# Kernel optimization log

Measured on AMD Instinct MI355X. Metric: run time of the kernel, lower is better.

The kernel has to match this reference:

```python
import jax, jax.numpy as jnp
import numpy as np

B, T, U = 64, 400, 64
V, E, H = 80, 128, 400
M, K = 10, 20  # attention mixtures, output mixtures


def _lstm_cell(x, h, c, W_ih, W_hh, b_ih, b_hh):
    g = x @ W_ih.T + b_ih + h @ W_hh.T + b_hh
    i, f, gg, o = jnp.split(g, 4, axis=-1)
    c_new = jax.nn.sigmoid(f) * c + jax.nn.sigmoid(i) * jnp.tanh(gg)
    h_new = jax.nn.sigmoid(o) * jnp.tanh(c_new)
    return h_new, c_new


def setup_inputs() -> dict:
    key = jax.random.key(0)
    ks = jax.random.split(key, 16)
    s = 0.05
    inp = {
        'strokes': jax.random.normal(ks[0], (B, T, 3), jnp.float32),
        'chars': jax.random.randint(ks[1], (B, U), 0, V, jnp.int32),
        'chars_mask': jnp.ones((B, U), jnp.float32),
        'emb': jax.random.normal(ks[2], (V, E)) * s,
        # layer_0: input 3+E
        'W_ih0': jax.random.normal(ks[3], (4 * H, 3 + E)) * s,
        'W_hh0': jax.random.normal(ks[4], (4 * H, H)) * s,
        'b_ih0': jnp.zeros((4 * H,)), 'b_hh0': jnp.zeros((4 * H,)),
        # layer_n[0], layer_n[1]: input 3+E+H
        'W_ih1': jax.random.normal(ks[5], (4 * H, 3 + E + H)) * s,
        'W_hh1': jax.random.normal(ks[6], (4 * H, H)) * s,
        'b_ih1': jnp.zeros((4 * H,)), 'b_hh1': jnp.zeros((4 * H,)),
        'W_ih2': jax.random.normal(ks[7], (4 * H, 3 + E + H)) * s,
        'W_hh2': jax.random.normal(ks[8], (4 * H, H)) * s,
        'b_ih2': jnp.zeros((4 * H,)), 'b_hh2': jnp.zeros((4 * H,)),
        # Gaussian attention linear: H -> 3M
        'Wa': jax.random.normal(ks[9], (3 * M, H)) * s,
        'ba': jnp.zeros((3 * M,)),
        # output linear: 3H -> 6K+1
        'Wo': jax.random.normal(ks[10], (6 * K + 1, 3 * H)) * s,
        'bo': jnp.zeros((6 * K + 1,)),
        # learned initial states
        'h0': jnp.zeros((3, H)), 'c0': jnp.zeros((3, H)),
        'w0': jnp.zeros((E,)), 'k0': jnp.zeros((M,)),
    }
    return inp


def _forward(strokes, chars, chars_mask, emb, W_ih0, W_hh0, b_ih0, b_hh0,
             W_ih1, W_hh1, b_ih1, b_hh1, W_ih2, W_hh2, b_ih2, b_hh2,
             Wa, ba, Wo, bo, h0, c0, w0, k0):
    ctx = emb[chars] * chars_mask[:, :, None]            # (B,U,E)
    u = jnp.arange(U, dtype=jnp.float32)                 # (U,)
    bsz = strokes.shape[0]

    def attn(h_t, k_tm1):
        p = jnp.exp(h_t @ Wa.T + ba)                     # (B,3M)
        alpha, beta, kappa = jnp.split(p, 3, axis=-1)    # (B,M) each
        kappa = kappa + k_tm1
        # phi: (B,U)
        phi = jnp.sum(alpha[:, None, :] * jnp.exp(-beta[:, None, :]
                      * (kappa[:, None, :] - u[None, :, None]) ** 2), axis=-1)
        w = jnp.sum(phi[:, :, None] * ctx, axis=1)       # (B,E)
        return w, kappa

    bc = lambda v: jnp.broadcast_to(v, (bsz,) + v.shape)
    carry0 = (bc(h0[0]), bc(h0[1]), bc(h0[2]),
              bc(c0[0]), bc(c0[1]), bc(c0[2]), bc(w0), bc(k0))

    def step(carry, x_t):
        h0_, h1_, h2_, c0_, c1_, c2_, w_, k_ = carry
        # layer_0
        hA, cA = _lstm_cell(jnp.concatenate([x_t, w_], 1), h0_, c0_,
                            W_ih0, W_hh0, b_ih0, b_hh0)
        w_n, k_n = attn(hA, k_)
        # faithful replication of source's buggy layer_n loop (j starts at 0):
        # j=0: input uses h_tm1[-1] (slot2), prev state = slot1, writes slot0
        n0h, n0c = _lstm_cell(jnp.concatenate([x_t, w_n, h2_], 1), h1_, c1_,
                              W_ih1, W_hh1, b_ih1, b_hh1)
        # j=1: input uses h_tm1[0] (just written), prev state = slot2, writes slot1
        n1h, n1c = _lstm_cell(jnp.concatenate([x_t, w_n, n0h], 1), h2_, c2_,
                              W_ih2, W_hh2, b_ih2, b_hh2)
        # slot2 never updated; output uses [slot0, slot1, slot2]
        out = jnp.concatenate([n0h, n1h, h2_], 1) @ Wo.T + bo
        return (n0h, n1h, h2_, n0c, n1c, c2_, w_n, k_n), out

    _, outs = jax.lax.scan(step, carry0, jnp.swapaxes(strokes, 0, 1))
    out = jnp.swapaxes(outs, 0, 1)                       # (B,T,6K+1)

    mu, log_sigma, pi, rho_raw, eos = jnp.split(
        out, [2 * K, 4 * K, 5 * K, 6 * K], axis=-1)
    sigma = jnp.exp(log_sigma).reshape(out.shape[0], out.shape[1], K, 2)
    mu = mu.reshape(out.shape[0], out.shape[1], K, 2)
    rho = jnp.tanh(rho_raw)                              # (B,T,K)
    log_pi = jax.nn.log_softmax(pi, axis=-1)

    x = strokes[:, :, None, :2]                          # (B,T,1,2)
    t = (x - mu) / sigma                                 # (B,T,K,2)
    Z = jnp.sum(t ** 2, -1) - 2.0 * rho * t[..., 0] * t[..., 1]
    num = -Z / (2.0 * (1.0 - rho ** 2))
    denom = (np.log(2 * np.pi) + jnp.sum(jnp.log(sigma), -1)
             + 0.5 * jnp.log(1.0 - rho ** 2))
    log_N = num - denom
    stroke_loss = jnp.mean(-jax.nn.logsumexp(log_pi + log_N, axis=-1))

    y = strokes[:, :, 2:3]
    z = eos
    eos_loss = jnp.mean(jnp.maximum(z, 0.0) - z * y
                        + jnp.log1p(jnp.exp(-jnp.abs(z))))
    return jnp.stack([stroke_loss, eos_loss])


def reference(strokes, chars, chars_mask, emb, W_ih0, W_hh0, b_ih0, b_hh0,
              W_ih1, W_hh1, b_ih1, b_hh1, W_ih2, W_hh2, b_ih2, b_hh2,
              Wa, ba, Wo, bo, h0, c0, w0, k0):
    return _forward(strokes, chars, chars_mask, emb, W_ih0, W_hh0, b_ih0,
                    b_hh0, W_ih1, W_hh1, b_ih1, b_hh1, W_ih2, W_hh2, b_ih2,
                    b_hh2, Wa, ba, Wo, bo, h0, c0, w0, k0)
```

## Files before the change

kernel.cpp:

```cpp
#include <hip/hip_runtime.h>
#include <hip/hip_bf16.h>


#define B_ 64
#define T_ 400
#define U_ 64
#define E_ 128
#define H_ 400
#define M_ 10
#define NO_ 121

#define NBLK 100
#define NTHR 512

constexpr size_t OF_WS2  = 128;
constexpr size_t OF_KS   = OF_WS2 + 64*128;
constexpr size_t OF_N0H  = OF_KS + 640;
constexpr size_t OF_N0C  = OF_N0H + 25600;
constexpr size_t OF_N1H  = OF_N0C + 25600;
constexpr size_t OF_N1C  = OF_N1H + 25600;
constexpr size_t OF_HA   = OF_N1C + 25600;
constexpr size_t OF_B0   = OF_HA + 25600;
constexpr size_t OF_B1   = OF_B0 + 1600;
constexpr size_t OF_B2   = OF_B1 + 1600;
constexpr size_t OF_OB   = OF_B2 + 1600;
constexpr size_t OF_XT   = OF_OB + 128;
constexpr size_t OF_CTX  = OF_XT + (size_t)T_*3*64;
constexpr size_t OF_A0   = OF_CTX + (size_t)64*64*128;
constexpr size_t OF_A1   = OF_A0 + (size_t)T_*64*400/2;
constexpr size_t WS_FLOATS = OF_A1 + (size_t)T_*64*400/2;

__device__ __forceinline__ float sigf(float x) { return 1.f/(1.f + expf(-x)); }

__device__ __forceinline__ void gbar(unsigned* cnt, unsigned* gen, unsigned tgt) {
  __syncthreads();
  if (threadIdx.x == 0) {
    unsigned prev = __hip_atomic_fetch_add(cnt, 1u, __ATOMIC_RELEASE, __HIP_MEMORY_SCOPE_AGENT);
    if (prev == tgt*(unsigned)NBLK - 1u) {
      __hip_atomic_store(gen, tgt, __ATOMIC_RELEASE, __HIP_MEMORY_SCOPE_AGENT);
    } else {
      while (__hip_atomic_load(gen, __ATOMIC_RELAXED, __HIP_MEMORY_SCOPE_AGENT) < tgt)
        __builtin_amdgcn_s_sleep(2);
    }
    __builtin_amdgcn_fence(__ATOMIC_ACQUIRE, "agent");
  }
  __syncthreads();
}

__global__ void k_pre(
  const float* __restrict__ strokes, const int* __restrict__ chars, const float* __restrict__ cmask,
  const float* __restrict__ emb,
  const float* __restrict__ Wih1, const float* __restrict__ Whh2, const float* __restrict__ Wo,
  const float* __restrict__ bih0, const float* __restrict__ bhh0,
  const float* __restrict__ bih1, const float* __restrict__ bhh1,
  const float* __restrict__ bih2, const float* __restrict__ bhh2,
  const float* __restrict__ bo,
  const float* __restrict__ h0, const float* __restrict__ c0,
  const float* __restrict__ w0, const float* __restrict__ k0,
  float* __restrict__ ws)
{
  const int gid = blockIdx.x*blockDim.x + threadIdx.x;
  const int gsz = gridDim.x*blockDim.x;
  float* ctxp = ws + OF_CTX;
  for (int i = gid; i < 64*64*128; i += gsz) {
    int b = i >> 13, rem = i & 8191, u = rem >> 7, e = rem & 127;
    ctxp[i] = emb[chars[b*64+u]*128+e] * cmask[b*64+u];
  }
  float* xT = ws + OF_XT;
  for (int i = gid; i < T_*3*64; i += gsz) {
    int t = i/192, r = i - t*192, j = r >> 6, b = r & 63;
    xT[i] = strokes[(b*T_+t)*3+j];
  }
  const float* h2c = h0 + 800;
  float* b0 = ws + OF_B0; float* b1 = ws + OF_B1; float* b2 = ws + OF_B2;
  for (int r = gid; r < 1600; r += gsz) {
    b0[r] = bih0[r] + bhh0[r];
    float s1 = bih1[r] + bhh1[r];
    const float* w1 = Wih1 + (size_t)r*531 + 131;
    for (int j = 0; j < 400; ++j) s1 += w1[j]*h2c[j];
    b1[r] = s1;
    float s2 = bih2[r] + bhh2[r];
    const float* w2 = Whh2 + (size_t)r*400;
    for (int j = 0; j < 400; ++j) s2 += w2[j]*h2c[j];
    b2[r] = s2;
  }
  float* ob = ws + OF_OB;
  for (int r = gid; r < 121; r += gsz) {
    float s = bo[r];
    const float* wr = Wo + (size_t)r*1200 + 800;
    for (int j = 0; j < 400; ++j) s += wr[j]*h2c[j];
    ob[r] = s;
  }
  float* wS = ws + OF_WS2;
  for (int i = gid; i < 8192; i += gsz) wS[i] = w0[i & 127];
  float* kS = ws + OF_KS;
  for (int i = gid; i < 640; i += gsz) kS[i] = k0[i % 10];
  float* n1hp = ws + OF_N1H; float* n1cp = ws + OF_N1C;
  for (int i = gid; i < 25600; i += gsz) {
    n1hp[i] = h0[400 + (i % 400)];
    n1cp[i] = c0[400 + (i >> 6)];
  }
}

__global__ __launch_bounds__(512) void k_init(
  const float* __restrict__ Wih0, const float* __restrict__ Whh0,
  const float* __restrict__ h0, const float* __restrict__ c0, const float* __restrict__ w0,
  float* __restrict__ ws)
{
  const int lane = threadIdx.x & 63;
  const int wv = threadIdx.x >> 6;
  const int n = blockIdx.x*8 + wv;
  if (n >= 400) return;
  const float* bias0 = ws + OF_B0;
  const float* xT = ws + OF_XT;
  float* hA = ws + OF_HA;
  float g[4];
  #pragma unroll
  for (int q = 0; q < 4; ++q) {
    int r = q*400 + n;
    const float* wi = Wih0 + (size_t)r*131;
    const float* wh = Whh0 + (size_t)r*400;
    float a = bias0[r];
    a += xT[0*64+lane]*wi[0] + xT[1*64+lane]*wi[1] + xT[2*64+lane]*wi[2];
    for (int e = 0; e < 128; ++e) a += w0[e]*wi[3+e];
    for (int j = 0; j < 400; ++j) a += h0[j]*wh[j];
    g[q] = a;
  }
  float cn = sigf(g[1])*c0[n] + sigf(g[0])*tanhf(g[2]);
  hA[lane*400 + n] = sigf(g[3])*tanhf(cn);
}

__device__ __forceinline__ void gemv8(
    int xt_idx, int lane, int kq, int rh, int ns, int ch,
    const float* __restrict__ bias,
    const float* __restrict__ Wxw, int sxw,
    const float* __restrict__ Whh, int shh, int hoff,
    const float* __restrict__ xT,
    const float* hLs, const float* wLs, float* pLs)
{
  const int hrows = 2*ch;
  float acc[8]; const float* wrow[8];
  #pragma unroll
  for (int s = 0; s < 8; ++s) {
    if (s < hrows) {
      int rr = rh*hrows + s;
      int q = rr / ch, nl = rr - q*ch;
      int r = __builtin_amdgcn_readfirstlane(q*H_ + ns + nl);
      if (kq == 0) { wrow[s] = Wxw + (size_t)r*sxw;        acc[s] = bias[r]; }
      else         { wrow[s] = Whh + (size_t)r*shh + hoff; acc[s] = 0.f; }
    }
  }
  if (kq == 0) {
    float x0 = xT[(xt_idx*3+0)*64+lane];
    float x1 = xT[(xt_idx*3+1)*64+lane];
    float x2 = xT[(xt_idx*3+2)*64+lane];
    #pragma unroll
    for (int s = 0; s < 8; ++s) if (s < hrows)
      acc[s] += x0*wrow[s][0] + x1*wrow[s][1] + x2*wrow[s][2];
    #pragma unroll 2
    for (int ec = 0; ec < 32; ++ec) {
      float4 w4 = *(const float4*)&wLs[lane*132 + ec*4];
      #pragma unroll
      for (int s = 0; s < 8; ++s) if (s < hrows) {
        const float* wp = wrow[s] + 3 + ec*4;
        acc[s] += w4.x*wp[0] + w4.y*wp[1] + w4.z*wp[2] + w4.w*wp[3];
      }
    }
  } else {
    int jb = (kq==1) ? 0 : (kq==2 ? 33 : 66);
    int je = (kq==1) ? 33 : (kq==2 ? 66 : 100);
    #pragma unroll 2
    for (int jc = jb; jc < je; ++jc) {
      float4 hv = *(const float4*)&hLs[lane*404 + jc*4];
      #pragma unroll
      for (int s = 0; s < 8; ++s) if (s < hrows) {
        const float* wp = wrow[s] + jc*4;
        acc[s] += hv.x*wp[0] + hv.y*wp[1] + hv.z*wp[2] + hv.w*wp[3];
      }
    }
  }
  #pragma unroll
  for (int s = 0; s < 8; ++s) if (s < hrows)
    pLs[((rh*4+kq)*8 + s)*64 + lane] = acc[s];
}

__global__ __launch_bounds__(NTHR) void k_scan(
  const float* __restrict__ Wih0, const float* __restrict__ Whh0,
  const float* __restrict__ Wih1, const float* __restrict__ Whh1,
  const float* __restrict__ Wih2,
  const float* __restrict__ Wa, const float* __restrict__ ba,
  const float* __restrict__ c0, float* __restrict__ ws)
{
  __shared__ __align__(16) float hLs[64*404];
  __shared__ __align__(16) float wLs[64*132];
  __shared__ float pLs[8*8*64];
  __shared__ float hab[400];
  __shared__ float pA[240];
  __shared__ float aScr[32];
  __shared__ float phL[64];

  const int tid = threadIdx.x;
  const int lane = tid & 63;
  const int wv = __builtin_amdgcn_readfirstlane(tid >> 6);
  const int kq = wv & 3, rh = wv >> 2;
  const int bid = blockIdx.x;
  const int ns = bid*4;

  unsigned* ctrl = (unsigned*)ws;
  unsigned* cnt = &ctrl[0];
  unsigned* gen = &ctrl[32];
  float* wS  = ws + OF_WS2;
  float* kS  = ws + OF_KS;
  float* n0h = ws + OF_N0H; float* n0c = ws + OF_N0C;
  float* n1h = ws + OF_N1H; float* n1c = ws + OF_N1C;
  float* hA  = ws + OF_HA;
  const float* bias0 = ws + OF_B0;
  const float* bias1 = ws + OF_B1;
  const float* bias2 = ws + OF_B2;
  const float* xT  = ws + OF_XT;
  const float* ctx = ws + OF_CTX;
  __hip_bfloat16* a0 = (__hip_bfloat16*)(ws + OF_A0);
  __hip_bfloat16* a1 = (__hip_bfloat16*)(ws + OF_A1);

  unsigned bgen = 0;

  for (int t = 0; t < T_; ++t) {
    if (bid < 64) {
      const int b = bid;
      for (int i = tid; i < 400; i += NTHR) hab[i] = hA[b*400+i];
      __syncthreads();
      if (tid < 240) {
        int r = tid >> 3, seg = tid & 7;
        const float* wr = Wa + r*400 + seg*50;
        const float* hb = hab + seg*50;
        float s = 0.f;
        for (int j = 0; j < 50; ++j) s += hb[j]*wr[j];
        pA[tid] = s;
      }
      __syncthreads();
      if (tid < 30) {
        float s = ba[tid];
        #pragma unroll
        for (int seg = 0; seg < 8; ++seg) s += pA[tid*8+seg];
        float p = expf(s);
        if (tid < 20) aScr[tid] = p;
        else { int m = tid-20; float kn = p + kS[b*10+m]; kS[b*10+m] = kn; aScr[tid] = kn; }
      }
      __syncthreads();
      if (tid < 64) {
        float u = (float)tid, ph = 0.f;
        #pragma unroll
        for (int m = 0; m < 10; ++m) { float d = aScr[20+m]-u; ph += aScr[m]*expf(-aScr[10+m]*d*d); }
        phL[tid] = ph;
      }
      __syncthreads();
      if (tid < 128) {
        float a = 0.f;
        const float* cb = ctx + ((size_t)b*64)*128 + tid;
        for (int u = 0; u < 64; ++u) a += phL[u]*cb[(size_t)u*128];
        wS[b*128+tid] = a;
      }
    }
    for (int i = tid; i < 6400; i += NTHR) {
      int b = i/100, jc = i - b*100;
      *(float4*)&hLs[b*404+jc*4] = *(const float4*)&n1h[b*400+jc*4];
    }
    gbar(cnt, gen, ++bgen);

    for (int i = tid; i < 2048; i += NTHR) {
      int b = i/32, ec = i - b*32;
      *(float4*)&wLs[b*132+ec*4] = *(const float4*)&wS[b*128+ec*4];
    }
    __syncthreads();
    gemv8(t, lane, kq, rh, ns, 4, bias1, Wih1, 531, Whh1, 400, 0, xT, hLs, wLs, pLs);
    __syncthreads();
    for (int i = tid; i < 256; i += NTHR) {
      int nl = i >> 6, b = i & 63, n = ns+nl;
      float g[4];
      #pragma unroll
      for (int q = 0; q < 4; ++q) {
        int rr = q*4+nl; int r2 = (rr >= 8); int s = rr - r2*8;
        float v = 0.f;
        #pragma unroll
        for (int k2 = 0; k2 < 4; ++k2) v += pLs[((r2*4+k2)*8+s)*64+b];
        g[q] = v;
      }
      float cp = n1c[n*64+b];
      float cn = sigf(g[1])*cp + sigf(g[0])*tanhf(g[2]);
      float hn = sigf(g[3])*tanhf(cn);
      n0c[n*64+b] = cn;
      n0h[b*400+n] = hn;
      a0[((size_t)t*64+b)*400+n] = __float2bfloat16(hn);
    }
    gbar(cnt, gen, ++bgen);

    for (int i = tid; i < 6400; i += NTHR) {
      int b = i/100, jc = i - b*100;
      *(float4*)&hLs[b*404+jc*4] = *(const float4*)&n0h[b*400+jc*4];
    }
    __syncthreads();
    gemv8(t, lane, kq, rh, ns, 4, bias2, Wih2, 531, Wih2, 531, 131, xT, hLs, wLs, pLs);
    __syncthreads();
    for (int i = tid; i < 256; i += NTHR) {
      int nl = i >> 6, b = i & 63, n = ns+nl;
      float g[4];
      #pragma unroll
      for (int q = 0; q < 4; ++q) {
        int rr = q*4+nl; int r2 = (rr >= 8); int s = rr - r2*8;
        float v = 0.f;
        #pragma unroll
        for (int k2 = 0; k2 < 4; ++k2) v += pLs[((r2*4+k2)*8+s)*64+b];
        g[q] = v;
      }
      float cn = sigf(g[1])*c0[800+n] + sigf(g[0])*tanhf(g[2]);
      float hn = sigf(g[3])*tanhf(cn);
      n1c[n*64+b] = cn;
      n1h[b*400+n] = hn;
      a1[((size_t)t*64+b)*400+n] = __float2bfloat16(hn);
    }
    __syncthreads();
    if (t < T_-1) {
      gemv8(t+1, lane, kq, rh, ns, 4, bias0, Wih0, 131, Whh0, 400, 0, xT, hLs, wLs, pLs);
      __syncthreads();
      for (int i = tid; i < 256; i += NTHR) {
        int nl = i >> 6, b = i & 63, n = ns+nl;
        float g[4];
        #pragma unroll
        for (int q = 0; q < 4; ++q) {
          int rr = q*4+nl; int r2 = (rr >= 8); int s = rr - r2*8;
          float v = 0.f;
          #pragma unroll
          for (int k2 = 0; k2 < 4; ++k2) v += pLs[((r2*4+k2)*8+s)*64+b];
          g[q] = v;
        }
        float cp = n0c[n*64+b];
        float cn = sigf(g[1])*cp + sigf(g[0])*tanhf(g[2]);
        hA[b*400+n] = sigf(g[3])*tanhf(cn);
      }
    }
    gbar(cnt, gen, ++bgen);
  }
}

__global__ __launch_bounds__(NTHR) void k_outloss(
  const float* __restrict__ Wo, const float* __restrict__ strokes, float* __restrict__ ws)
{
  __shared__ __align__(16) float hL4[64*404];
  __shared__ float oL[121*65];
  const int t = blockIdx.x;
  const int tid = threadIdx.x;
  const int lane = tid & 63;
  const int wv = __builtin_amdgcn_readfirstlane(tid >> 6);
  const float* ob = ws + OF_OB;
  const __hip_bfloat16* a0 = (const __hip_bfloat16*)(ws + OF_A0);
  const __hip_bfloat16* a1 = (const __hip_bfloat16*)(ws + OF_A1);

  float acc[16];
  #pragma unroll
  for (int s = 0; s < 16; ++s) { int r = wv + 8*s; acc[s] = (r < 121) ? ob[r] : 0.f; }

  const unsigned* src0 = (const unsigned*)(a0 + (size_t)t*25600);
  for (int i = tid; i < 12800; i += NTHR) {
    unsigned v = src0[i];
    int b = i/200, jc = i - b*200;
    hL4[b*404+jc*2+0] = __uint_as_float(v << 16);
    hL4[b*404+jc*2+1] = __uint_as_float(v & 0xffff0000u);
  }
  __syncthreads();
  for (int jc = 0; jc < 100; ++jc) {
    float4 hv = *(const float4*)&hL4[lane*404+jc*4];
    #pragma unroll
    for (int s = 0; s < 16; ++s) {
      int r = wv + 8*s;
      if (r < 121) {
        const float* wp = Wo + (size_t)r*1200 + jc*4;
        acc[s] += hv.x*wp[0] + hv.y*wp[1] + hv.z*wp[2] + hv.w*wp[3];
      }
    }
  }
  __syncthreads();
  const unsigned* src1 = (const unsigned*)(a1 + (size_t)t*25600);
  for (int i = tid; i < 12800; i += NTHR) {
    unsigned v = src1[i];
    int b = i/200, jc = i - b*200;
    hL4[b*404+jc*2+0] = __uint_as_float(v << 16);
    hL4[b*404+jc*2+1] = __uint_as_float(v & 0xffff0000u);
  }
  __syncthreads();
  for (int jc = 0; jc < 100; ++jc) {
    float4 hv = *(const float4*)&hL4[lane*404+jc*4];
    #pragma unroll
    for (int s = 0; s < 16; ++s) {
      int r = wv + 8*s;
      if (r < 121) {
        const float* wp = Wo + (size_t)r*1200 + 400 + jc*4;
        acc[s] += hv.x*wp[0] + hv.y*wp[1] + hv.z*wp[2] + hv.w*wp[3];
      }
    }
  }
  #pragma unroll
  for (int s = 0; s < 16; ++s) { int r = wv + 8*s; if (r < 121) oL[r*65+lane] = acc[s]; }
  __syncthreads();

  if (wv == 0) {
    const int b = lane;
    float x0 = strokes[(b*T_+t)*3+0];
    float x1 = strokes[(b*T_+t)*3+1];
    float y  = strokes[(b*T_+t)*3+2];
    float mp = -1e30f;
    #pragma unroll
    for (int k = 0; k < 20; ++k) mp = fmaxf(mp, oL[(80+k)*65+b]);
    float sp = 0.f;
    #pragma unroll
    for (int k = 0; k < 20; ++k) sp += expf(oL[(80+k)*65+b] - mp);
    float lsep = mp + logf(sp);
    float sk[20]; float ms = -1e30f;
    #pragma unroll
    for (int k = 0; k < 20; ++k) {
      float mu0 = oL[(2*k)*65+b],    mu1 = oL[(2*k+1)*65+b];
      float l0  = oL[(40+2*k)*65+b], l1  = oL[(41+2*k)*65+b];
      float rho = tanhf(oL[(100+k)*65+b]);
      float t0 = (x0-mu0)*expf(-l0);
      float t1 = (x1-mu1)*expf(-l1);
      float on = 1.f - rho*rho;
      float Z = t0*t0 + t1*t1 - 2.f*rho*t0*t1;
      float logN = -Z/(2.f*on) - (1.8378770664093453f + l0 + l1 + 0.5f*logf(on));
      float sv = (oL[(80+k)*65+b] - lsep) + logN;
      sk[k] = sv; ms = fmaxf(ms, sv);
    }
    float ss = 0.f;
    #pragma unroll
    for (int k = 0; k < 20; ++k) ss += expf(sk[k]-ms);
    float stroke = -(ms + logf(ss));
    float z = oL[120*65+b];
    float eos = fmaxf(z,0.f) - z*y + log1pf(expf(-fabsf(z)));
    #pragma unroll
    for (int off = 32; off > 0; off >>= 1) {
      stroke += __shfl_down(stroke, off, 64);
      eos    += __shfl_down(eos, off, 64);
    }
    if (lane == 0) { atomicAdd(ws+64, stroke); atomicAdd(ws+65, eos); }
  }
}

__global__ void k_fin(const float* __restrict__ ws, float* __restrict__ out) {
  if (threadIdx.x == 0) {
    out[0] = ws[64] * (1.f/25600.f);
    out[1] = ws[65] * (1.f/25600.f);
  }
}

extern "C" void kernel_launch(void* const* d_in, const int* in_sizes, int n_in,
                              void* d_out, int out_size, void* d_ws, size_t ws_size,
                              hipStream_t stream) {
  const float* strokes = (const float*)d_in[0];
  const int*   chars   = (const int*)d_in[1];
  const float* cmask   = (const float*)d_in[2];
  const float* emb     = (const float*)d_in[3];
  const float* Wih0    = (const float*)d_in[4];
  const float* Whh0    = (const float*)d_in[5];
  const float* bih0    = (const float*)d_in[6];
  const float* bhh0    = (const float*)d_in[7];
  const float* Wih1    = (const float*)d_in[8];
  const float* Whh1    = (const float*)d_in[9];
  const float* bih1    = (const float*)d_in[10];
  const float* bhh1    = (const float*)d_in[11];
  const float* Wih2    = (const float*)d_in[12];
  const float* Whh2    = (const float*)d_in[13];
  const float* bih2    = (const float*)d_in[14];
  const float* bhh2    = (const float*)d_in[15];
  const float* Wa      = (const float*)d_in[16];
  const float* ba      = (const float*)d_in[17];
  const float* Wo      = (const float*)d_in[18];
  const float* bo      = (const float*)d_in[19];
  const float* h0      = (const float*)d_in[20];
  const float* c0      = (const float*)d_in[21];
  const float* w0      = (const float*)d_in[22];
  const float* k0      = (const float*)d_in[23];
  float* ws = (float*)d_ws;
  float* out = (float*)d_out;
  if (ws_size < WS_FLOATS*sizeof(float)) return;

  hipMemsetAsync(d_ws, 0, 512, stream);
  k_pre<<<256, 256, 0, stream>>>(strokes, chars, cmask, emb, Wih1, Whh2, Wo,
                                 bih0, bhh0, bih1, bhh1, bih2, bhh2, bo,
                                 h0, c0, w0, k0, ws);
  k_init<<<50, 512, 0, stream>>>(Wih0, Whh0, h0, c0, w0, ws);
  k_scan<<<NBLK, NTHR, 0, stream>>>(Wih0, Whh0, Wih1, Whh1, Wih2, Wa, ba, c0, ws);
  k_outloss<<<T_, NTHR, 0, stream>>>(Wo, strokes, ws);
  k_fin<<<1, 64, 0, stream>>>(ws, out);
}
```

Before: 33.74 ms.

## Relax grid barrier ordering and run attention in one wavefront with device-scope accesses

Drops the release/acquire ordering and the acquire fence from the software grid barrier. Cross-block shared state (hidden states, attention window) is now read and written with relaxed agent-scope atomic loads and stores, which avoid stale non-coherent caches without the fence. The attention step collapses into a single wavefront that avoids block-wide syncs, while the other wavefronts load n1h into LDS at the same time. The risk is memory-ordering correctness, because relaxed atomics plus a relaxed counter may not guarantee visibility, and loads narrow from float4 to float2.

New measurement: 41.35 ms. 1.23x slower.

```diff
diff --git a/kernel.cpp b/kernel.cpp
--- a/kernel.cpp
+++ b/kernel.cpp
@@ -32,17 +32,28 @@
 
 __device__ __forceinline__ float sigf(float x) { return 1.f/(1.f + expf(-x)); }
 
+__device__ __forceinline__ float ld_dev(const float* p) {
+  unsigned v = __hip_atomic_load((const unsigned*)p, __ATOMIC_RELAXED, __HIP_MEMORY_SCOPE_AGENT);
+  return __uint_as_float(v);
+}
+__device__ __forceinline__ float2 ld_dev2(const float* p) {
+  unsigned long long v = __hip_atomic_load((const unsigned long long*)p, __ATOMIC_RELAXED, __HIP_MEMORY_SCOPE_AGENT);
+  union { unsigned long long u; float2 f; } c; c.u = v; return c.f;
+}
+__device__ __forceinline__ void st_dev(float* p, float v) {
+  __hip_atomic_store((unsigned*)p, __float_as_uint(v), __ATOMIC_RELAXED, __HIP_MEMORY_SCOPE_AGENT);
+}
+
 __device__ __forceinline__ void gbar(unsigned* cnt, unsigned* gen, unsigned tgt) {
   __syncthreads();
   if (threadIdx.x == 0) {
-    unsigned prev = __hip_atomic_fetch_add(cnt, 1u, __ATOMIC_RELEASE, __HIP_MEMORY_SCOPE_AGENT);
+    unsigned prev = __hip_atomic_fetch_add(cnt, 1u, __ATOMIC_RELAXED, __HIP_MEMORY_SCOPE_AGENT);
     if (prev == tgt*(unsigned)NBLK - 1u) {
-      __hip_atomic_store(gen, tgt, __ATOMIC_RELEASE, __HIP_MEMORY_SCOPE_AGENT);
+      __hip_atomic_store(gen, tgt, __ATOMIC_RELAXED, __HIP_MEMORY_SCOPE_AGENT);
     } else {
       while (__hip_atomic_load(gen, __ATOMIC_RELAXED, __HIP_MEMORY_SCOPE_AGENT) < tgt)
-        __builtin_amdgcn_s_sleep(2);
-    }
-    __builtin_amdgcn_fence(__ATOMIC_ACQUIRE, "agent");
+        __builtin_amdgcn_s_sleep(4);
+    }
   }
   __syncthreads();
 }
@@ -195,7 +206,6 @@
   __shared__ __align__(16) float wLs[64*132];
   __shared__ float pLs[8*8*64];
   __shared__ float hab[400];
-  __shared__ float pA[240];
   __shared__ float aScr[32];
   __shared__ float phL[64];
 
@@ -226,50 +236,66 @@
 
   for (int t = 0; t < T_; ++t) {
     if (bid < 64) {
-      const int b = bid;
-      for (int i = tid; i < 400; i += NTHR) hab[i] = hA[b*400+i];
-      __syncthreads();
-      if (tid < 240) {
-        int r = tid >> 3, seg = tid & 7;
-        const float* wr = Wa + r*400 + seg*50;
-        const float* hb = hab + seg*50;
+      if (wv == 0) {
+        const int b = bid;
+        for (int i = lane; i < 200; i += 64) {
+          float2 v = ld_dev2(&hA[b*400 + i*2]);
+          *(float2*)&hab[i*2] = v;
+        }
+        asm volatile("s_waitcnt vmcnt(0) lgkmcnt(0)" ::: "memory");
         float s = 0.f;
-        for (int j = 0; j < 50; ++j) s += hb[j]*wr[j];
-        pA[tid] = s;
-      }
-      __syncthreads();
-      if (tid < 30) {
-        float s = ba[tid];
+        if (lane < 30) {
+          const float* wr = Wa + lane*400;
+          #pragma unroll 4
+          for (int j = 0; j < 400; ++j) s += hab[j]*wr[j];
+          s += ba[lane];
+        }
+        float p = expf(s);
+        float val = p;
+        if (lane >= 20 && lane < 30) {
+          float kap = p + kS[b*10 + (lane-20)];
+          kS[b*10 + (lane-20)] = kap;
+          val = kap;
+        }
+        if (lane < 30) aScr[lane] = val;
+        asm volatile("s_waitcnt lgkmcnt(0)" ::: "memory");
+        float uu = (float)lane, ph = 0.f;
         #pragma unroll
-        for (int seg = 0; seg < 8; ++seg) s += pA[tid*8+seg];
-        float p = expf(s);
-        if (tid < 20) aScr[tid] = p;
-        else { int m = tid-20; float kn = p + kS[b*10+m]; kS[b*10+m] = kn; aScr[tid] = kn; }
-      }
-      __syncthreads();
-      if (tid < 64) {
-        float u = (float)tid, ph = 0.f;
-        #pragma unroll
-        for (int m = 0; m < 10; ++m) { float d = aScr[20+m]-u; ph += aScr[m]*expf(-aScr[10+m]*d*d); }
-        phL[tid] = ph;
-      }
-      __syncthreads();
-      if (tid < 128) {
-        float a = 0.f;
-        const float* cb = ctx + ((size_t)b*64)*128 + tid;
-        for (int u = 0; u < 64; ++u) a += phL[u]*cb[(size_t)u*128];
-        wS[b*128+tid] = a;
-      }
-    }
-    for (int i = tid; i < 6400; i += NTHR) {
-      int b = i/100, jc = i - b*100;
-      *(float4*)&hLs[b*404+jc*4] = *(const float4*)&n1h[b*400+jc*4];
+        for (int m = 0; m < 10; ++m) {
+          float d = aScr[20+m] - uu;
+          ph += aScr[m] * expf(-aScr[10+m]*d*d);
+        }
+        phL[lane] = ph;
+        asm volatile("s_waitcnt lgkmcnt(0)" ::: "memory");
+        float a0w = 0.f, a1w = 0.f;
+        const float* cb = ctx + (size_t)b*8192;
+        for (int u2 = 0; u2 < 64; ++u2) {
+          float phv = phL[u2];
+          a0w += phv * cb[u2*128 + lane];
+          a1w += phv * cb[u2*128 + 64 + lane];
+        }
+        st_dev(&wS[b*128 + lane], a0w);
+        st_dev(&wS[b*128 + 64 + lane], a1w);
+      } else {
+        for (int i = tid - 64; i < 12800; i += (NTHR-64)) {
+          int b2 = i/200, jc = i - b2*200;
+          float2 v = ld_dev2(&n1h[b2*400 + jc*2]);
+          *(float2*)&hLs[b2*404 + jc*2] = v;
+        }
+      }
+    } else {
+      for (int i = tid; i < 12800; i += NTHR) {
+        int b2 = i/200, jc = i - b2*200;
+        float2 v = ld_dev2(&n1h[b2*400 + jc*2]);
+        *(float2*)&hLs[b2*404 + jc*2] = v;
+      }
     }
     gbar(cnt, gen, ++bgen);
 
-    for (int i = tid; i < 2048; i += NTHR) {
-      int b = i/32, ec = i - b*32;
-      *(float4*)&wLs[b*132+ec*4] = *(const float4*)&wS[b*128+ec*4];
+    for (int i = tid; i < 4096; i += NTHR) {
+      int b2 = i >> 6, ec = i & 63;
+      float2 v = ld_dev2(&wS[b2*128 + ec*2]);
+      *(float2*)&wLs[b2*132 + ec*2] = v;
     }
     __syncthreads();
     gemv8(t, lane, kq, rh, ns, 4, bias1, Wih1, 531, Whh1, 400, 0, xT, hLs, wLs, pLs);
@@ -289,14 +315,15 @@
       float cn = sigf(g[1])*cp + sigf(g[0])*tanhf(g[2]);
       float hn = sigf(g[3])*tanhf(cn);
       n0c[n*64+b] = cn;
-      n0h[b*400+n] = hn;
+      st_dev(&n0h[b*400+n], hn);
       a0[((size_t)t*64+b)*400+n] = __float2bfloat16(hn);
     }
     gbar(cnt, gen, ++bgen);
 
-    for (int i = tid; i < 6400; i += NTHR) {
-      int b = i/100, jc = i - b*100;
-      *(float4*)&hLs[b*404+jc*4] = *(const float4*)&n0h[b*400+jc*4];
+    for (int i = tid; i < 12800; i += NTHR) {
+      int b2 = i/200, jc = i - b2*200;
+      float2 v = ld_dev2(&n0h[b2*400 + jc*2]);
+      *(float2*)&hLs[b2*404 + jc*2] = v;
     }
     __syncthreads();
     gemv8(t, lane, kq, rh, ns, 4, bias2, Wih2, 531, Wih2, 531, 131, xT, hLs, wLs, pLs);
@@ -315,7 +342,7 @@
       float cn = sigf(g[1])*c0[800+n] + sigf(g[0])*tanhf(g[2]);
       float hn = sigf(g[3])*tanhf(cn);
       n1c[n*64+b] = cn;
-      n1h[b*400+n] = hn;
+      st_dev(&n1h[b*400+n], hn);
       a1[((size_t)t*64+b)*400+n] = __float2bfloat16(hn);
     }
     __syncthreads();
@@ -335,7 +362,7 @@
         }
         float cp = n0c[n*64+b];
         float cn = sigf(g[1])*cp + sigf(g[0])*tanhf(g[2]);
-        hA[b*400+n] = sigf(g[3])*tanhf(cn);
+        st_dev(&hA[b*400+n], sigf(g[3])*tanhf(cn));
       }
     }
     gbar(cnt, gen, ++bgen);
```
